# Optimization experiments

Measured on AMD Instinct MI355X. Metric: run time of the kernel, lower is better.

The kernel has to match this reference:

```python
import jax, jax.numpy as jnp
import numpy as np

B, T, C = 4, 2048, 1024
N_HEAD = 16
D_HEAD = C // N_HEAD


def setup_inputs() -> dict:
    key = jax.random.key(0)
    ks = jax.random.split(key, 5)
    s_in = 1.0 / np.sqrt(C)
    return {
        "x": jax.random.normal(ks[0], (B, T, C), dtype=jnp.float32),
        "Wqkv": jax.random.uniform(ks[1], (C, 3 * C), dtype=jnp.float32, minval=-s_in, maxval=s_in),
        "bqkv": jax.random.uniform(ks[2], (3 * C,), dtype=jnp.float32, minval=-s_in, maxval=s_in),
        "Wproj": jax.random.uniform(ks[3], (C, C), dtype=jnp.float32, minval=-s_in, maxval=s_in),
        "bproj": jax.random.uniform(ks[4], (C,), dtype=jnp.float32, minval=-s_in, maxval=s_in),
    }


def reference(x, Wqkv, bqkv, Wproj, bproj):
    b, t, c = x.shape
    qkv = x @ Wqkv + bqkv                      # [B,T,3C]
    q, k, v = jnp.split(qkv, 3, axis=2)
    # [B,T,H,Dh] -> [B,H,T,Dh]
    q = q.reshape(b, t, N_HEAD, D_HEAD).transpose(0, 2, 1, 3)
    k = k.reshape(b, t, N_HEAD, D_HEAD).transpose(0, 2, 1, 3)
    v = v.reshape(b, t, N_HEAD, D_HEAD).transpose(0, 2, 1, 3)
    scale = 1.0 / np.sqrt(D_HEAD).astype(np.float32)
    att = jnp.einsum("bhqd,bhkd->bhqk", q, k) * scale   # [B,H,T,T]
    causal = jnp.tril(jnp.ones((t, t), dtype=bool))
    att = jnp.where(causal, att, jnp.float32(-jnp.inf))
    att = jax.nn.softmax(att, axis=-1)
    y = jnp.einsum("bhqk,bhkd->bhqd", att, v)            # [B,H,T,Dh]
    y = y.transpose(0, 2, 1, 3).reshape(b, t, c)
    return y @ Wproj + bproj
```

## Files before the change

kernel.cpp:

```cpp
#include <hip/hip_runtime.h>

using u16 = unsigned short;
typedef __attribute__((ext_vector_type(8))) __bf16 bf16x8;
typedef __attribute__((ext_vector_type(4))) float f32x4;
typedef __attribute__((ext_vector_type(16))) float f32x16;
typedef __attribute__((ext_vector_type(4))) unsigned int u32x4;
typedef __attribute__((ext_vector_type(2))) unsigned int u32x2;

__device__ inline u16 f2bf(float f) {
    unsigned u = __float_as_uint(f);
    u += 0x7FFFu + ((u >> 16) & 1u);
    return (u16)(u >> 16);
}
__device__ inline unsigned pack2(float a, float b) {
    return (unsigned)f2bf(a) | ((unsigned)f2bf(b) << 16);
}
__device__ inline bf16x8 as_bf16x8(u32x4 v) {
    union { u32x4 u; bf16x8 b; } x; x.u = v; return x.b;
}
__device__ inline unsigned cvtpk(float lo, float hi) {
    unsigned w;
    asm("v_cvt_pk_bf16_f32 %0, %1, %2" : "=v"(w) : "v"(lo), "v"(hi));
    return w;
}
__device__ inline void gload_lds16(const void* g, void* l) {
    __builtin_amdgcn_global_load_lds(
        (const __attribute__((address_space(1))) void*)g,
        (__attribute__((address_space(3))) void*)l, 16, 0, 0);
}

__global__ __launch_bounds__(256) void xcast(const float* __restrict__ in,
                                             u16* __restrict__ out) {
    const size_t i = ((size_t)blockIdx.x * 256 + threadIdx.x) * 8;
    f32x4 a = *(const f32x4*)(in + i);
    f32x4 b = *(const f32x4*)(in + i + 4);
    u32x4 w;
    w[0] = pack2(a[0], a[1]); w[1] = pack2(a[2], a[3]);
    w[2] = pack2(b[0], b[1]); w[3] = pack2(b[2], b[3]);
    *(u32x4*)(out + i) = w;
}

__global__ __launch_bounds__(256) void tcast_f32(const float* __restrict__ in,
                                                 u16* __restrict__ out,
                                                 int R, int C) {
    __shared__ float tile[64][65];
    const int r0 = blockIdx.x * 64, c0 = blockIdx.y * 64;
    const int t = threadIdx.x;
    {
        const int r = t >> 2, cq = (t & 3) * 16;
        const float* src = in + (size_t)(r0 + r) * C + c0 + cq;
#pragma unroll
        for (int j = 0; j < 4; ++j) {
            f32x4 v = *(const f32x4*)(src + j * 4);
#pragma unroll
            for (int e = 0; e < 4; ++e) tile[r][cq + j * 4 + e] = v[e];
        }
    }
    __syncthreads();
    {
        const int c = t >> 2, rq = (t & 3) * 16;
        u32x4 w0, w1;
#pragma unroll
        for (int j = 0; j < 4; ++j) {
            w0[j] = pack2(tile[rq + 2 * j][c], tile[rq + 2 * j + 1][c]);
            w1[j] = pack2(tile[rq + 8 + 2 * j][c], tile[rq + 8 + 2 * j + 1][c]);
        }
        u16* dst = out + (size_t)(c0 + c) * R + r0 + rq;
        *(u32x4*)dst = w0;
        *(u32x4*)(dst + 8) = w1;
    }
}

__global__ __launch_bounds__(256) void tv_bf16(const u16* __restrict__ V,
                                               u16* __restrict__ Vt) {
    __shared__ u16 tile[64][68];
    const int t0 = blockIdx.x * 64, bh = blockIdx.y;
    const int t = threadIdx.x;
    {
        const int r = t >> 2, cq = (t & 3) * 16;
        const u16* src = V + ((size_t)bh * 2048 + t0 + r) * 64 + cq;
        u32x4 a = *(const u32x4*)src;
        u32x4 b = *(const u32x4*)(src + 8);
#pragma unroll
        for (int j = 0; j < 4; ++j) {
            tile[r][cq + 2 * j] = (u16)(a[j] & 0xFFFFu);
            tile[r][cq + 2 * j + 1] = (u16)(a[j] >> 16);
            tile[r][cq + 8 + 2 * j] = (u16)(b[j] & 0xFFFFu);
            tile[r][cq + 8 + 2 * j + 1] = (u16)(b[j] >> 16);
        }
    }
    __syncthreads();
    {
        const int d = t >> 2, rq = (t & 3) * 16;
        u32x4 w0, w1;
#pragma unroll
        for (int j = 0; j < 4; ++j) {
            w0[j] = (unsigned)tile[rq + 2 * j][d] | ((unsigned)tile[rq + 2 * j + 1][d] << 16);
            w1[j] = (unsigned)tile[rq + 8 + 2 * j][d] | ((unsigned)tile[rq + 8 + 2 * j + 1][d] << 16);
        }
        u16* dst = Vt + ((size_t)bh * 64 + d) * 2048 + t0 + rq;
        *(u32x4*)dst = w0;
        *(u32x4*)(dst + 8) = w1;
    }
}

template <int EPI>
__global__ __launch_bounds__(256) void gemm_kernel(const u16* __restrict__ A,
                                                   const u16* __restrict__ Bt,
                                                   const float* __restrict__ bias,
                                                   void* __restrict__ outp,
                                                   const int M, const int N, const int K) {
    __shared__ char lds[16384];
    char* As = lds;
    char* Bs = lds + 8192;
    const int t = threadIdx.x;
    const int l = t & 63, wid = t >> 6;
    const int wr = wid >> 1, wc = wid & 1;
    const int g = l >> 4, lr = l & 15;
    const int m0 = blockIdx.x * 128, n0 = blockIdx.y * 128;

    f32x4 acc[4][4];
#pragma unroll
    for (int i = 0; i < 4; ++i)
#pragma unroll
        for (int j = 0; j < 4; ++j)
#pragma unroll
            for (int e = 0; e < 4; ++e) acc[i][j][e] = 0.f;

    const int srow = l >> 2;
    const int sby = (l & 3) * 16;
    const size_t Kb2 = (size_t)K * 2;

    for (int k0 = 0; k0 < K; k0 += 32) {
        const size_t kb = (size_t)k0 * 2 + sby;
#pragma unroll
        for (int j = 0; j < 2; ++j) {
            const int row = j * 64 + wid * 16 + srow;
            gload_lds16((const char*)A + (size_t)(m0 + row) * Kb2 + kb,
                        As + j * 4096 + wid * 1024);
            gload_lds16((const char*)Bt + (size_t)(n0 + row) * Kb2 + kb,
                        Bs + j * 4096 + wid * 1024);
        }
        __syncthreads();
        bf16x8 a[4], b[4];
#pragma unroll
        for (int m = 0; m < 4; ++m) {
            const int row = wr * 64 + m * 16 + lr;
            a[m] = as_bf16x8(*(const u32x4*)(As + row * 64 + g * 16));
        }
#pragma unroll
        for (int n = 0; n < 4; ++n) {
            const int row = wc * 64 + n * 16 + lr;
            b[n] = as_bf16x8(*(const u32x4*)(Bs + row * 64 + g * 16));
        }
        __builtin_amdgcn_s_setprio(1);
#pragma unroll
        for (int m = 0; m < 4; ++m)
#pragma unroll
            for (int n = 0; n < 4; ++n)
                acc[m][n] = __builtin_amdgcn_mfma_f32_16x16x32_bf16(a[m], b[n], acc[m][n], 0, 0, 0);
        __builtin_amdgcn_s_setprio(0);
        __syncthreads();
    }

#pragma unroll
    for (int m = 0; m < 4; ++m) {
#pragma unroll
        for (int n = 0; n < 4; ++n) {
            const int colg = n0 + wc * 64 + n * 16 + lr;
            const float bv = bias[colg];
#pragma unroll
            for (int r = 0; r < 4; ++r) {
                const int rowg = m0 + wr * 64 + m * 16 + g * 4 + r;
                const float v = acc[m][n][r] + bv;
                if constexpr (EPI == 0) {
                    const int sec = colg >> 10, c = colg & 1023;
                    const int hh = c >> 6, dd = c & 63;
                    const int bb = rowg >> 11, tt = rowg & 2047;
                    u16* dst = (u16*)outp;
                    dst[(size_t)sec * 8388608u +
                        (((size_t)(bb * 16 + hh) * 2048 + tt) << 6) + dd] = f2bf(v);
                } else {
                    ((float*)outp)[(size_t)rowg * N + colg] = v;
                }
            }
        }
    }
}

__global__ __launch_bounds__(512) void attn_kernel(const u16* __restrict__ Q,
                                                   const u16* __restrict__ K,
                                                   const u16* __restrict__ Vt,
                                                   u16* __restrict__ Y) {
    __shared__ char lds[65536];
    const int t = threadIdx.x;
    const int l = t & 63, w = t >> 6;
    const int q = l & 31, hi = l >> 5;
    const int bh = blockIdx.y;
    const char* Kby = (const char*)(K + (size_t)bh * 131072);
    const char* Vby = (const char*)(Vt + (size_t)bh * 131072);
    const u16* Qb = Q + (size_t)bh * 131072;
    const int bb = bh >> 4, hh = bh & 15;
    const float c = 0.18033688f;
    const int sr = w * 8 + (l >> 3);
    const unsigned ck = (unsigned)(((l & 7) ^ (l >> 3)) << 4);
    const unsigned rd_swz = (unsigned)((q & 7) << 4);

#pragma unroll 1
    for (int job = 0; job < 2; ++job) {
        const int p = job ? (7 - (int)blockIdx.x) : (int)blockIdx.x;
        const int q0w = p * 256 + w * 32;
        const int qg = q0w + q;
        const int NT = 4 * p + 4;
        const int ntw = ((q0w + 31) >> 6) + 1;

        bf16x8 qf[4];
#pragma unroll
        for (int ks = 0; ks < 4; ++ks)
            qf[ks] = as_bf16x8(*(const u32x4*)(Qb + (size_t)(q0w + q) * 64 + ks * 16 + hi * 8));

        f32x16 o0, o1;
#pragma unroll
        for (int r = 0; r < 16; ++r) { o0[r] = 0.f; o1[r] = 0.f; }
        float M = -3.0e38f, lsum = 0.f;

        auto STAGE = [&](int it, int b) {
            const int kv0 = it << 6;
            char* base = lds + b * 16384;
            gload_lds16(Kby + (size_t)(kv0 + sr) * 128 + ck, base + w * 1024);
            gload_lds16(Vby + (size_t)sr * 4096 + (size_t)kv0 * 2 + ck,
                        base + 8192 + w * 1024);
        };

        STAGE(0, 0); STAGE(1, 1); STAGE(2, 2);
#pragma unroll 1
        for (int it = 0; it < NT; ++it) {
            if (it + 2 < NT)      asm volatile("s_waitcnt vmcnt(4)" ::: "memory");
            else if (it + 1 < NT) asm volatile("s_waitcnt vmcnt(2)" ::: "memory");
            else                  asm volatile("s_waitcnt vmcnt(0)" ::: "memory");
            __builtin_amdgcn_s_barrier();
            if (it + 3 < NT) STAGE(it + 3, (it + 3) & 3);
            if (it < ntw) {
                const int kv0 = it << 6;
                const char* Kl = lds + (it & 3) * 16384;
                const char* Vl = Kl + 8192;
                u32x4 vf[8];
#pragma unroll
                for (int kvb = 0; kvb < 2; ++kvb)
#pragma unroll
                    for (int s = 0; s < 2; ++s)
#pragma unroll
                        for (int db = 0; db < 2; ++db)
                            vf[kvb * 4 + s * 2 + db] = *(const u32x4*)(
                                Vl + (unsigned)((db * 32 + q) * 128) +
                                ((unsigned)(kvb * 64 + s * 32 + hi * 16) ^ rd_swz));
                f32x16 s0, s1;
#pragma unroll
                for (int r = 0; r < 16; ++r) { s0[r] = 0.f; s1[r] = 0.f; }
                __builtin_amdgcn_s_setprio(1);
#pragma unroll
                for (int ks = 0; ks < 4; ++ks) {
                    const unsigned co = (unsigned)(ks * 32 + hi * 16) ^ rd_swz;
                    bf16x8 kf0 = as_bf16x8(*(const u32x4*)(Kl + (unsigned)(q * 128) + co));
                    s0 = __builtin_amdgcn_mfma_f32_32x32x16_bf16(kf0, qf[ks], s0, 0, 0, 0);
                    bf16x8 kf1 = as_bf16x8(*(const u32x4*)(Kl + (unsigned)((32 + q) * 128) + co));
                    s1 = __builtin_amdgcn_mfma_f32_32x32x16_bf16(kf1, qf[ks], s1, 0, 0, 0);
                }
                __builtin_amdgcn_s_setprio(0);
                if (kv0 + 63 > q0w) {
#pragma unroll
                    for (int r = 0; r < 16; ++r) {
                        const int roff = (r & 3) + 8 * (r >> 2) + hi * 4;
                        if (kv0 + roff > qg) s0[r] = -1.0e30f;
                        if (kv0 + 32 + roff > qg) s1[r] = -1.0e30f;
                    }
                }
                float mx[8];
#pragma unroll
                for (int j = 0; j < 8; ++j)
                    mx[j] = fmaxf(fmaxf(s0[2 * j], s0[2 * j + 1]),
                                  fmaxf(s1[2 * j], s1[2 * j + 1]));
                float pmax = fmaxf(fmaxf(fmaxf(mx[0], mx[1]), fmaxf(mx[2], mx[3])),
                                   fmaxf(fmaxf(mx[4], mx[5]), fmaxf(mx[6], mx[7])));
                {
                    u32x2 rr = __builtin_amdgcn_permlane32_swap(
                        __float_as_uint(pmax), __float_as_uint(pmax), false, false);
                    pmax = fmaxf(pmax, __uint_as_float(hi ? rr[0] : rr[1]));
                }
                if (__any(pmax > M + 55.0f)) {
                    const float Mn = fmaxf(M, pmax);
                    const float al = exp2f((M - Mn) * c);
                    M = Mn;
                    lsum *= al;
#pragma unroll
                    for (int r = 0; r < 16; ++r) {
                        const float alq = __shfl(al, (r & 3) + 8 * (r >> 2) + hi * 4);
                        o0[r] *= alq;
                        o1[r] *= alq;
                    }
                }
                const float mc = M * c;
                float sm[8];
#pragma unroll
                for (int j = 0; j < 8; ++j) {
                    s0[2 * j]     = exp2f(fmaf(s0[2 * j],     c, -mc));
                    s0[2 * j + 1] = exp2f(fmaf(s0[2 * j + 1], c, -mc));
                    s1[2 * j]     = exp2f(fmaf(s1[2 * j],     c, -mc));
                    s1[2 * j + 1] = exp2f(fmaf(s1[2 * j + 1], c, -mc));
                    sm[j] = (s0[2 * j] + s0[2 * j + 1]) + (s1[2 * j] + s1[2 * j + 1]);
                }
                float psum = ((sm[0] + sm[1]) + (sm[2] + sm[3])) +
                             ((sm[4] + sm[5]) + (sm[6] + sm[7]));
                {
                    u32x2 rr = __builtin_amdgcn_permlane32_swap(
                        __float_as_uint(psum), __float_as_uint(psum), false, false);
                    psum += __uint_as_float(hi ? rr[0] : rr[1]);
                }
                lsum += psum;
#pragma unroll
                for (int kvb = 0; kvb < 2; ++kvb) {
                    unsigned wd[8];
#pragma unroll
                    for (int j = 0; j < 8; ++j) {
                        const float plo = kvb ? s1[2 * j] : s0[2 * j];
                        const float phi = kvb ? s1[2 * j + 1] : s0[2 * j + 1];
                        wd[j] = cvtpk(plo, phi);
                    }
                    u32x2 r0 = __builtin_amdgcn_permlane32_swap(wd[0], wd[2], false, false);
                    u32x2 r1 = __builtin_amdgcn_permlane32_swap(wd[1], wd[3], false, false);
                    u32x2 r2 = __builtin_amdgcn_permlane32_swap(wd[4], wd[6], false, false);
                    u32x2 r3 = __builtin_amdgcn_permlane32_swap(wd[5], wd[7], false, false);
                    u32x4 fa, fb;
                    fa[0] = r0[0]; fa[1] = r1[0]; fa[2] = r0[1]; fa[3] = r1[1];
                    fb[0] = r2[0]; fb[1] = r3[0]; fb[2] = r2[1]; fb[3] = r3[1];
                    const bf16x8 pa = as_bf16x8(fa), pb = as_bf16x8(fb);
                    __builtin_amdgcn_s_setprio(1);
                    o0 = __builtin_amdgcn_mfma_f32_32x32x16_bf16(pa, as_bf16x8(vf[kvb * 4 + 0]), o0, 0, 0, 0);
                    o1 = __builtin_amdgcn_mfma_f32_32x32x16_bf16(pa, as_bf16x8(vf[kvb * 4 + 1]), o1, 0, 0, 0);
                    o0 = __builtin_amdgcn_mfma_f32_32x32x16_bf16(pb, as_bf16x8(vf[kvb * 4 + 2]), o0, 0, 0, 0);
                    o1 = __builtin_amdgcn_mfma_f32_32x32x16_bf16(pb, as_bf16x8(vf[kvb * 4 + 3]), o1, 0, 0, 0);
                    __builtin_amdgcn_s_setprio(0);
                }
            }
        }
        const float linv = 1.f / lsum;
#pragma unroll
        for (int r = 0; r < 16; ++r) {
            const int roff = (r & 3) + 8 * (r >> 2) + hi * 4;
            const float invq = __shfl(linv, roff);
            const size_t base = ((size_t)(bb * 2048 + q0w + roff)) * 1024 + hh * 64 + q;
            Y[base] = f2bf(o0[r] * invq);
            Y[base + 32] = f2bf(o1[r] * invq);
        }
    }
}

extern "C" void kernel_launch(void* const* d_in, const int* in_sizes, int n_in,
                              void* d_out, int out_size, void* d_ws, size_t ws_size,
                              hipStream_t stream) {
    const float* x = (const float*)d_in[0];
    const float* Wqkv = (const float*)d_in[1];
    const float* bqkv = (const float*)d_in[2];
    const float* Wproj = (const float*)d_in[3];
    const float* bproj = (const float*)d_in[4];
    float* out = (float*)d_out;
    char* ws = (char*)d_ws;

    u16* Wtq = (u16*)(ws + 0);
    u16* Wtp = (u16*)(ws + 6291456);
    u16* Qb  = (u16*)(ws + 8388608);
    u16* Vb  = (u16*)(ws + 41943040);
    u16* Vtb = (u16*)(ws + 58720256);
    u16* Xb  = (u16*)(ws + 58720256);
    u16* Yb  = Vb;

    xcast<<<4096, 256, 0, stream>>>(x, Xb);
    tcast_f32<<<dim3(16, 48), 256, 0, stream>>>(Wqkv, Wtq, 1024, 3072);
    tcast_f32<<<dim3(16, 16), 256, 0, stream>>>(Wproj, Wtp, 1024, 1024);
    gemm_kernel<0><<<dim3(64, 24), 256, 0, stream>>>(
        Xb, Wtq, bqkv, (void*)Qb, 8192, 3072, 1024);
    tv_bf16<<<dim3(32, 64), 256, 0, stream>>>(Vb, Vtb);
    attn_kernel<<<dim3(4, 64), 512, 0, stream>>>(
        Qb, Qb + 8388608, Vtb, Yb);
    gemm_kernel<1><<<dim3(64, 8), 256, 0, stream>>>(
        Yb, Wtp, bproj, (void*)out, 8192, 1024, 1024);
}
```

Measured before the change: 195.2 us.

## Pipeline GEMM K-loop with triple-buffered async loads and remap blocks across XCDs

Measured after the change: 247.7 us. +26.9%, slower.

```diff
diff --git a/kernel.cpp b/kernel.cpp
--- a/kernel.cpp
+++ b/kernel.cpp
@@ -110,14 +110,16 @@
                                                    const float* __restrict__ bias,
                                                    void* __restrict__ outp,
                                                    const int M, const int N, const int K) {
-    __shared__ char lds[16384];
-    char* As = lds;
-    char* Bs = lds + 8192;
+    __shared__ char lds[49152];
     const int t = threadIdx.x;
     const int l = t & 63, wid = t >> 6;
     const int wr = wid >> 1, wc = wid & 1;
     const int g = l >> 4, lr = l & 15;
-    const int m0 = blockIdx.x * 128, n0 = blockIdx.y * 128;
+    const int gx = gridDim.x;
+    const int id = blockIdx.y * gx + blockIdx.x;
+    const int cpx = (gx * gridDim.y) >> 3;
+    const int virt = (id & 7) * cpx + (id >> 3);
+    const int m0 = (virt % gx) * 128, n0 = (virt / gx) * 128;
 
     f32x4 acc[4][4];
 #pragma unroll
@@ -127,21 +129,32 @@
 #pragma unroll
             for (int e = 0; e < 4; ++e) acc[i][j][e] = 0.f;
 
-    const int srow = l >> 2;
-    const int sby = (l & 3) * 16;
     const size_t Kb2 = (size_t)K * 2;
-
-    for (int k0 = 0; k0 < K; k0 += 32) {
-        const size_t kb = (size_t)k0 * 2 + sby;
+    const size_t rowbA = (size_t)(m0 + wid * 16 + (l >> 2)) * Kb2 + (l & 3) * 16;
+    const size_t rowbB = (size_t)(n0 + wid * 16 + (l >> 2)) * Kb2 + (l & 3) * 16;
+    const int kn = K >> 5;
+
+    auto STAGE = [&](int kk) {
+        char* buf = lds + (kk % 3) * 16384;
+        const size_t kb = (size_t)kk * 64;
 #pragma unroll
         for (int j = 0; j < 2; ++j) {
-            const int row = j * 64 + wid * 16 + srow;
-            gload_lds16((const char*)A + (size_t)(m0 + row) * Kb2 + kb,
-                        As + j * 4096 + wid * 1024);
-            gload_lds16((const char*)Bt + (size_t)(n0 + row) * Kb2 + kb,
-                        Bs + j * 4096 + wid * 1024);
-        }
-        __syncthreads();
+            gload_lds16((const char*)A + rowbA + j * 64 * Kb2 + kb,
+                        buf + j * 4096 + wid * 1024);
+            gload_lds16((const char*)Bt + rowbB + j * 64 * Kb2 + kb,
+                        buf + 8192 + j * 4096 + wid * 1024);
+        }
+    };
+
+    STAGE(0); STAGE(1);
+#pragma unroll 1
+    for (int kk = 0; kk < kn; ++kk) {
+        if (kk + 1 < kn) asm volatile("s_waitcnt vmcnt(4)" ::: "memory");
+        else             asm volatile("s_waitcnt vmcnt(0)" ::: "memory");
+        __builtin_amdgcn_s_barrier();
+        if (kk + 2 < kn) STAGE(kk + 2);
+        const char* As = lds + (kk % 3) * 16384;
+        const char* Bs = As + 8192;
         bf16x8 a[4], b[4];
 #pragma unroll
         for (int m = 0; m < 4; ++m) {
@@ -160,7 +173,6 @@
             for (int n = 0; n < 4; ++n)
                 acc[m][n] = __builtin_amdgcn_mfma_f32_16x16x32_bf16(a[m], b[n], acc[m][n], 0, 0, 0);
         __builtin_amdgcn_s_setprio(0);
-        __syncthreads();
     }
 
 #pragma unroll
@@ -188,170 +200,172 @@
     }
 }
 
-__global__ __launch_bounds__(512) void attn_kernel(const u16* __restrict__ Q,
+__global__ __launch_bounds__(256) void attn_kernel(const u16* __restrict__ Q,
                                                    const u16* __restrict__ K,
                                                    const u16* __restrict__ Vt,
                                                    u16* __restrict__ Y) {
-    __shared__ char lds[65536];
+    __shared__ char lds[49152];
     const int t = threadIdx.x;
     const int l = t & 63, w = t >> 6;
     const int q = l & 31, hi = l >> 5;
-    const int bh = blockIdx.y;
+    const int id = (int)blockIdx.y * 16 + (int)blockIdx.x;
+    const int virt = (id & 7) * 128 + (id >> 3);
+    const int bh = virt >> 4;
+    const int p = 15 - (virt & 15);
     const char* Kby = (const char*)(K + (size_t)bh * 131072);
     const char* Vby = (const char*)(Vt + (size_t)bh * 131072);
     const u16* Qb = Q + (size_t)bh * 131072;
     const int bb = bh >> 4, hh = bh & 15;
     const float c = 0.18033688f;
-    const int sr = w * 8 + (l >> 3);
     const unsigned ck = (unsigned)(((l & 7) ^ (l >> 3)) << 4);
     const unsigned rd_swz = (unsigned)((q & 7) << 4);
 
+    const int q0w = p * 128 + w * 32;
+    const int qg = q0w + q;
+    const int NT = 2 * p + 2;
+    const int ntw = ((q0w + 31) >> 6) + 1;
+
+    bf16x8 qf[4];
+#pragma unroll
+    for (int ks = 0; ks < 4; ++ks)
+        qf[ks] = as_bf16x8(*(const u32x4*)(Qb + (size_t)(q0w + q) * 64 + ks * 16 + hi * 8));
+
+    f32x16 o0, o1;
+#pragma unroll
+    for (int r = 0; r < 16; ++r) { o0[r] = 0.f; o1[r] = 0.f; }
+    float M = -3.0e38f, lsum = 0.f;
+
+    auto STAGE = [&](int it) {
+        const int kv0 = it << 6;
+        char* base = lds + (it % 3) * 16384;
+#pragma unroll
+        for (int j = 0; j < 2; ++j) {
+            const int r = w * 16 + j * 8 + (l >> 3);
+            gload_lds16(Kby + (size_t)(kv0 + r) * 128 + ck,
+                        base + w * 2048 + j * 1024);
+            gload_lds16(Vby + (size_t)r * 4096 + (size_t)kv0 * 2 + ck,
+                        base + 8192 + w * 2048 + j * 1024);
+        }
+    };
+
+    STAGE(0); STAGE(1);
 #pragma unroll 1
-    for (int job = 0; job < 2; ++job) {
-        const int p = job ? (7 - (int)blockIdx.x) : (int)blockIdx.x;
-        const int q0w = p * 256 + w * 32;
-        const int qg = q0w + q;
-        const int NT = 4 * p + 4;
-        const int ntw = ((q0w + 31) >> 6) + 1;
-
-        bf16x8 qf[4];
-#pragma unroll
-        for (int ks = 0; ks < 4; ++ks)
-            qf[ks] = as_bf16x8(*(const u32x4*)(Qb + (size_t)(q0w + q) * 64 + ks * 16 + hi * 8));
-
-        f32x16 o0, o1;
-#pragma unroll
-        for (int r = 0; r < 16; ++r) { o0[r] = 0.f; o1[r] = 0.f; }
-        float M = -3.0e38f, lsum = 0.f;
-
-        auto STAGE = [&](int it, int b) {
+    for (int it = 0; it < NT; ++it) {
+        if (it + 1 < NT) asm volatile("s_waitcnt vmcnt(4)" ::: "memory");
+        else             asm volatile("s_waitcnt vmcnt(0)" ::: "memory");
+        __builtin_amdgcn_s_barrier();
+        if (it + 2 < NT) STAGE(it + 2);
+        if (it < ntw) {
             const int kv0 = it << 6;
-            char* base = lds + b * 16384;
-            gload_lds16(Kby + (size_t)(kv0 + sr) * 128 + ck, base + w * 1024);
-            gload_lds16(Vby + (size_t)sr * 4096 + (size_t)kv0 * 2 + ck,
-                        base + 8192 + w * 1024);
-        };
-
-        STAGE(0, 0); STAGE(1, 1); STAGE(2, 2);
-#pragma unroll 1
-        for (int it = 0; it < NT; ++it) {
-            if (it + 2 < NT)      asm volatile("s_waitcnt vmcnt(4)" ::: "memory");
-            else if (it + 1 < NT) asm volatile("s_waitcnt vmcnt(2)" ::: "memory");
-            else                  asm volatile("s_waitcnt vmcnt(0)" ::: "memory");
-            __builtin_amdgcn_s_barrier();
-            if (it + 3 < NT) STAGE(it + 3, (it + 3) & 3);
-            if (it < ntw) {
-                const int kv0 = it << 6;
-                const char* Kl = lds + (it & 3) * 16384;
-                const char* Vl = Kl + 8192;
-                u32x4 vf[8];
-#pragma unroll
-                for (int kvb = 0; kvb < 2; ++kvb)
-#pragma unroll
-                    for (int s = 0; s < 2; ++s)
-#pragma unroll
-                        for (int db = 0; db < 2; ++db)
-                            vf[kvb * 4 + s * 2 + db] = *(const u32x4*)(
-                                Vl + (unsigned)((db * 32 + q) * 128) +
-                                ((unsigned)(kvb * 64 + s * 32 + hi * 16) ^ rd_swz));
-                f32x16 s0, s1;
-#pragma unroll
-                for (int r = 0; r < 16; ++r) { s0[r] = 0.f; s1[r] = 0.f; }
+            const char* Kl = lds + (it % 3) * 16384;
+            const char* Vl = Kl + 8192;
+            u32x4 vf[8];
+#pragma unroll
+            for (int kvb = 0; kvb < 2; ++kvb)
+#pragma unroll
+                for (int s = 0; s < 2; ++s)
+#pragma unroll
+                    for (int db = 0; db < 2; ++db)
+                        vf[kvb * 4 + s * 2 + db] = *(const u32x4*)(
+                            Vl + (unsigned)((db * 32 + q) * 128) +
+                            ((unsigned)(kvb * 64 + s * 32 + hi * 16) ^ rd_swz));
+            f32x16 s0, s1;
+#pragma unroll
+            for (int r = 0; r < 16; ++r) { s0[r] = 0.f; s1[r] = 0.f; }
+            __builtin_amdgcn_s_setprio(1);
+#pragma unroll
+            for (int ks = 0; ks < 4; ++ks) {
+                const unsigned co = (unsigned)(ks * 32 + hi * 16) ^ rd_swz;
+                bf16x8 kf0 = as_bf16x8(*(const u32x4*)(Kl + (unsigned)(q * 128) + co));
+                s0 = __builtin_amdgcn_mfma_f32_32x32x16_bf16(kf0, qf[ks], s0, 0, 0, 0);
+                bf16x8 kf1 = as_bf16x8(*(const u32x4*)(Kl + (unsigned)((32 + q) * 128) + co));
+                s1 = __builtin_amdgcn_mfma_f32_32x32x16_bf16(kf1, qf[ks], s1, 0, 0, 0);
+            }
+            __builtin_amdgcn_s_setprio(0);
+            if (kv0 + 63 > q0w) {
+#pragma unroll
+                for (int r = 0; r < 16; ++r) {
+                    const int roff = (r & 3) + 8 * (r >> 2) + hi * 4;
+                    if (kv0 + roff > qg) s0[r] = -1.0e30f;
+                    if (kv0 + 32 + roff > qg) s1[r] = -1.0e30f;
+                }
+            }
+            float mx[8];
+#pragma unroll
+            for (int j = 0; j < 8; ++j)
+                mx[j] = fmaxf(fmaxf(s0[2 * j], s0[2 * j + 1]),
+                              fmaxf(s1[2 * j], s1[2 * j + 1]));
+            float pmax = fmaxf(fmaxf(fmaxf(mx[0], mx[1]), fmaxf(mx[2], mx[3])),
+                               fmaxf(fmaxf(mx[4], mx[5]), fmaxf(mx[6], mx[7])));
+            {
+                u32x2 rr = __builtin_amdgcn_permlane32_swap(
+                    __float_as_uint(pmax), __float_as_uint(pmax), false, false);
+                pmax = fmaxf(pmax, __uint_as_float(hi ? rr[0] : rr[1]));
+            }
+            if (__any(pmax > M + 55.0f)) {
+                const float Mn = fmaxf(M, pmax);
+                const float al = exp2f((M - Mn) * c);
+                M = Mn;
+                lsum *= al;
+#pragma unroll
+                for (int r = 0; r < 16; ++r) {
+                    const float alq = __shfl(al, (r & 3) + 8 * (r >> 2) + hi * 4);
+                    o0[r] *= alq;
+                    o1[r] *= alq;
+                }
+            }
+            const float mc = M * c;
+            float sm[8];
+#pragma unroll
+            for (int j = 0; j < 8; ++j) {
+                s0[2 * j]     = exp2f(fmaf(s0[2 * j],     c, -mc));
+                s0[2 * j + 1] = exp2f(fmaf(s0[2 * j + 1], c, -mc));
+                s1[2 * j]     = exp2f(fmaf(s1[2 * j],     c, -mc));
+                s1[2 * j + 1] = exp2f(fmaf(s1[2 * j + 1], c, -mc));
+                sm[j] = (s0[2 * j] + s0[2 * j + 1]) + (s1[2 * j] + s1[2 * j + 1]);
+            }
+            float psum = ((sm[0] + sm[1]) + (sm[2] + sm[3])) +
+                         ((sm[4] + sm[5]) + (sm[6] + sm[7]));
+            {
+                u32x2 rr = __builtin_amdgcn_permlane32_swap(
+                    __float_as_uint(psum), __float_as_uint(psum), false, false);
+                psum += __uint_as_float(hi ? rr[0] : rr[1]);
+            }
+            lsum += psum;
+#pragma unroll
+            for (int kvb = 0; kvb < 2; ++kvb) {
+                unsigned wd[8];
+#pragma unroll
+                for (int j = 0; j < 8; ++j) {
+                    const float plo = kvb ? s1[2 * j] : s0[2 * j];
+                    const float phi = kvb ? s1[2 * j + 1] : s0[2 * j + 1];
+                    wd[j] = cvtpk(plo, phi);
+                }
+                u32x2 r0 = __builtin_amdgcn_permlane32_swap(wd[0], wd[2], false, false);
+                u32x2 r1 = __builtin_amdgcn_permlane32_swap(wd[1], wd[3], false, false);
+                u32x2 r2 = __builtin_amdgcn_permlane32_swap(wd[4], wd[6], false, false);
+                u32x2 r3 = __builtin_amdgcn_permlane32_swap(wd[5], wd[7], false, false);
+                u32x4 fa, fb;
+                fa[0] = r0[0]; fa[1] = r1[0]; fa[2] = r0[1]; fa[3] = r1[1];
+                fb[0] = r2[0]; fb[1] = r3[0]; fb[2] = r2[1]; fb[3] = r3[1];
+                const bf16x8 pa = as_bf16x8(fa), pb = as_bf16x8(fb);
                 __builtin_amdgcn_s_setprio(1);
-#pragma unroll
-                for (int ks = 0; ks < 4; ++ks) {
-                    const unsigned co = (unsigned)(ks * 32 + hi * 16) ^ rd_swz;
-                    bf16x8 kf0 = as_bf16x8(*(const u32x4*)(Kl + (unsigned)(q * 128) + co));
-                    s0 = __builtin_amdgcn_mfma_f32_32x32x16_bf16(kf0, qf[ks], s0, 0, 0, 0);
-                    bf16x8 kf1 = as_bf16x8(*(const u32x4*)(Kl + (unsigned)((32 + q) * 128) + co));
-                    s1 = __builtin_amdgcn_mfma_f32_32x32x16_bf16(kf1, qf[ks], s1, 0, 0, 0);
-                }
+                o0 = __builtin_amdgcn_mfma_f32_32x32x16_bf16(pa, as_bf16x8(vf[kvb * 4 + 0]), o0, 0, 0, 0);
+                o1 = __builtin_amdgcn_mfma_f32_32x32x16_bf16(pa, as_bf16x8(vf[kvb * 4 + 1]), o1, 0, 0, 0);
+                o0 = __builtin_amdgcn_mfma_f32_32x32x16_bf16(pb, as_bf16x8(vf[kvb * 4 + 2]), o0, 0, 0, 0);
+                o1 = __builtin_amdgcn_mfma_f32_32x32x16_bf16(pb, as_bf16x8(vf[kvb * 4 + 3]), o1, 0, 0, 0);
                 __builtin_amdgcn_s_setprio(0);
-                if (kv0 + 63 > q0w) {
-#pragma unroll
-                    for (int r = 0; r < 16; ++r) {
-                        const int roff = (r & 3) + 8 * (r >> 2) + hi * 4;
-                        if (kv0 + roff > qg) s0[r] = -1.0e30f;
-                        if (kv0 + 32 + roff > qg) s1[r] = -1.0e30f;
-                    }
-                }
-                float mx[8];
-#pragma unroll
-                for (int j = 0; j < 8; ++j)
-                    mx[j] = fmaxf(fmaxf(s0[2 * j], s0[2 * j + 1]),
-                                  fmaxf(s1[2 * j], s1[2 * j + 1]));
-                float pmax = fmaxf(fmaxf(fmaxf(mx[0], mx[1]), fmaxf(mx[2], mx[3])),
-                                   fmaxf(fmaxf(mx[4], mx[5]), fmaxf(mx[6], mx[7])));
-                {
-                    u32x2 rr = __builtin_amdgcn_permlane32_swap(
-                        __float_as_uint(pmax), __float_as_uint(pmax), false, false);
-                    pmax = fmaxf(pmax, __uint_as_float(hi ? rr[0] : rr[1]));
-                }
-                if (__any(pmax > M + 55.0f)) {
-                    const float Mn = fmaxf(M, pmax);
-                    const float al = exp2f((M - Mn) * c);
-                    M = Mn;
-                    lsum *= al;
-#pragma unroll
-                    for (int r = 0; r < 16; ++r) {
-                        const float alq = __shfl(al, (r & 3) + 8 * (r >> 2) + hi * 4);
-                        o0[r] *= alq;
-                        o1[r] *= alq;
-                    }
-                }
-                const float mc = M * c;
-                float sm[8];
-#pragma unroll
-                for (int j = 0; j < 8; ++j) {
-                    s0[2 * j]     = exp2f(fmaf(s0[2 * j],     c, -mc));
-                    s0[2 * j + 1] = exp2f(fmaf(s0[2 * j + 1], c, -mc));
-                    s1[2 * j]     = exp2f(fmaf(s1[2 * j],     c, -mc));
-                    s1[2 * j + 1] = exp2f(fmaf(s1[2 * j + 1], c, -mc));
-                    sm[j] = (s0[2 * j] + s0[2 * j + 1]) + (s1[2 * j] + s1[2 * j + 1]);
-                }
-                float psum = ((sm[0] + sm[1]) + (sm[2] + sm[3])) +
-                             ((sm[4] + sm[5]) + (sm[6] + sm[7]));
-                {
-                    u32x2 rr = __builtin_amdgcn_permlane32_swap(
-                        __float_as_uint(psum), __float_as_uint(psum), false, false);
-                    psum += __uint_as_float(hi ? rr[0] : rr[1]);
-                }
-                lsum += psum;
-#pragma unroll
-                for (int kvb = 0; kvb < 2; ++kvb) {
-                    unsigned wd[8];
-#pragma unroll
-                    for (int j = 0; j < 8; ++j) {
-                        const float plo = kvb ? s1[2 * j] : s0[2 * j];
-                        const float phi = kvb ? s1[2 * j + 1] : s0[2 * j + 1];
-                        wd[j] = cvtpk(plo, phi);
-                    }
-                    u32x2 r0 = __builtin_amdgcn_permlane32_swap(wd[0], wd[2], false, false);
-                    u32x2 r1 = __builtin_amdgcn_permlane32_swap(wd[1], wd[3], false, false);
-                    u32x2 r2 = __builtin_amdgcn_permlane32_swap(wd[4], wd[6], false, false);
-                    u32x2 r3 = __builtin_amdgcn_permlane32_swap(wd[5], wd[7], false, false);
-                    u32x4 fa, fb;
-                    fa[0] = r0[0]; fa[1] = r1[0]; fa[2] = r0[1]; fa[3] = r1[1];
-                    fb[0] = r2[0]; fb[1] = r3[0]; fb[2] = r2[1]; fb[3] = r3[1];
-                    const bf16x8 pa = as_bf16x8(fa), pb = as_bf16x8(fb);
-                    __builtin_amdgcn_s_setprio(1);
-                    o0 = __builtin_amdgcn_mfma_f32_32x32x16_bf16(pa, as_bf16x8(vf[kvb * 4 + 0]), o0, 0, 0, 0);
-                    o1 = __builtin_amdgcn_mfma_f32_32x32x16_bf16(pa, as_bf16x8(vf[kvb * 4 + 1]), o1, 0, 0, 0);
-                    o0 = __builtin_amdgcn_mfma_f32_32x32x16_bf16(pb, as_bf16x8(vf[kvb * 4 + 2]), o0, 0, 0, 0);
-                    o1 = __builtin_amdgcn_mfma_f32_32x32x16_bf16(pb, as_bf16x8(vf[kvb * 4 + 3]), o1, 0, 0, 0);
-                    __builtin_amdgcn_s_setprio(0);
-                }
-            }
-        }
-        const float linv = 1.f / lsum;
-#pragma unroll
-        for (int r = 0; r < 16; ++r) {
-            const int roff = (r & 3) + 8 * (r >> 2) + hi * 4;
-            const float invq = __shfl(linv, roff);
-            const size_t base = ((size_t)(bb * 2048 + q0w + roff)) * 1024 + hh * 64 + q;
-            Y[base] = f2bf(o0[r] * invq);
-            Y[base + 32] = f2bf(o1[r] * invq);
-        }
+            }
+        }
+    }
+    const float linv = 1.f / lsum;
+#pragma unroll
+    for (int r = 0; r < 16; ++r) {
+        const int roff = (r & 3) + 8 * (r >> 2) + hi * 4;
+        const float invq = __shfl(linv, roff);
+        const size_t base = ((size_t)(bb * 2048 + q0w + roff)) * 1024 + hh * 64 + q;
+        Y[base] = f2bf(o0[r] * invq);
+        Y[base + 32] = f2bf(o1[r] * invq);
     }
 }
 
@@ -380,7 +394,7 @@
     gemm_kernel<0><<<dim3(64, 24), 256, 0, stream>>>(
         Xb, Wtq, bqkv, (void*)Qb, 8192, 3072, 1024);
     tv_bf16<<<dim3(32, 64), 256, 0, stream>>>(Vb, Vtb);
-    attn_kernel<<<dim3(4, 64), 512, 0, stream>>>(
+    attn_kernel<<<dim3(16, 64), 256, 0, stream>>>(
         Qb, Qb + 8388608, Vtb, Yb);
     gemm_kernel<1><<<dim3(64, 8), 256, 0, stream>>>(
         Yb, Wtp, bproj, (void*)out, 8192, 1024, 1024);
```
